# Kernel tuning notes

Hardware: AMD Instinct MI355X
Metric: run time of the kernel (lower is better)

The kernel has to match this reference:

```python
import jax, jax.numpy as jnp
import numpy as np

EPS = 1e-06


def setup_inputs() -> dict:
    key = jax.random.key(0)
    kx, kw, kb = jax.random.split(key, 3)
    C = 128
    x = jax.random.normal(kx, (8, C, 256, 256), dtype=jnp.float32)
    # 1x1 conv weights: [C_out, C_in]
    W = jax.random.normal(kw, (C, C), dtype=jnp.float32) * (1.0 / np.sqrt(C))
    b = jax.random.normal(kb, (C,), dtype=jnp.float32) * 0.01
    return {"x": x, "W": W, "b": b}


def reference(x, W, b):
    # torch.std_mean over channel dim (dim=1), std is unbiased (ddof=1)
    u = jnp.mean(x, axis=1, keepdims=True)                  # [B,1,H,W]
    var = jnp.var(x, axis=1, keepdims=True, ddof=1)         # unbiased
    s = jnp.sqrt(var)
    n_x = (x - u) / (s + EPS)
    # 1x1 conv == pointwise GEMM over channels
    n_x = jnp.einsum('bchw,oc->bohw', n_x, W) + b[None, :, None, None]
    return x * n_x
```

## Files before the change

kernel.cpp:

```cpp
#include <hip/hip_runtime.h>

#define EPS 1e-6f

constexpr int C    = 128;
constexpr int HW   = 65536;
constexpr int TILE = 128;
constexpr int NT   = 512;

typedef __attribute__((ext_vector_type(8))) short bf16x8;
typedef __attribute__((ext_vector_type(4))) float f32x4;

__device__ __forceinline__ unsigned short f2bf(float f) {
    unsigned u = __float_as_uint(f);
    u += 0x7fff + ((u >> 16) & 1);
    return (unsigned short)(u >> 16);
}
__device__ __forceinline__ float bf2f(unsigned short u) {
    return __uint_as_float(((unsigned)u) << 16);
}
__device__ __forceinline__ unsigned pack2(float lo, float hi) {
    return (unsigned)f2bf(lo) | ((unsigned)f2bf(hi) << 16);
}

__global__ __launch_bounds__(NT, 4) void spnorm_kernel(
    const float* __restrict__ x, const float* __restrict__ W,
    const float* __restrict__ bias, float* __restrict__ out)
{
    __shared__ unsigned short bufT[C * TILE];
    __shared__ float red1[4][TILE], red2[4][TILE];
    __shared__ float u_s[TILE], se_s[TILE];

    const int tid = threadIdx.x;
    const int l   = tid & 63;
    const int wv  = tid >> 6;
    const int batch = blockIdx.x >> 9;
    const int hw0   = (blockIdx.x & 511) * TILE;
    const int base  = batch * (C * HW) + hw0;

    const int p = tid & 127;
    const int q = tid >> 7;

    float v[32];
    {
        const float* xp = x + base + q * 32 * HW + p;
        #pragma unroll
        for (int i = 0; i < 32; ++i)
            v[i] = xp[i * HW];
    }

    const int arow  = (wv << 4) + (l & 15);
    const int acol0 = (l >> 4) << 3;
    bf16x8 afrag[4];
    #pragma unroll
    for (int kk = 0; kk < 4; ++kk) {
        const float* wp = W + arow * C + kk * 32 + acol0;
        float4 wa = *reinterpret_cast<const float4*>(wp);
        float4 wb = *reinterpret_cast<const float4*>(wp + 4);
        bf16x8 f;
        f[0] = (short)f2bf(wa.x); f[1] = (short)f2bf(wa.y);
        f[2] = (short)f2bf(wa.z); f[3] = (short)f2bf(wa.w);
        f[4] = (short)f2bf(wb.x); f[5] = (short)f2bf(wb.y);
        f[6] = (short)f2bf(wb.z); f[7] = (short)f2bf(wb.w);
        afrag[kk] = f;
    }
    const int od = (wv << 4) + ((l >> 4) << 2);
    const f32x4 binit = { bias[od], bias[od + 1], bias[od + 2], bias[od + 3] };

    {
        float s1 = 0.f, s2 = 0.f;
        #pragma unroll
        for (int i = 0; i < 32; ++i) {
            s1 += v[i];
            s2 = fmaf(v[i], v[i], s2);
        }
        red1[q][p] = s1;
        red2[q][p] = s2;
    }
    __syncthreads();

    {
        float s1 = red1[0][p] + red1[1][p] + red1[2][p] + red1[3][p];
        float s2 = red2[0][p] + red2[1][p] + red2[2][p] + red2[3][p];
        float u   = s1 * (1.0f / 128.0f);
        float var = fmaxf((s2 - s1 * u) * (1.0f / 127.0f), 0.0f);
        float se  = sqrtf(var) + EPS;
        float iv  = 1.0f / se;
        if (q == 0) {
            u_s[p]  = u;
            se_s[p] = se;
        }
        char* tb = (char*)bufT;
        const int rowoff = p * 256;
        const int swz    = (p & 15) << 4;
        #pragma unroll
        for (int o8 = 0; o8 < 4; ++o8) {
            float n0 = (v[o8 * 8 + 0] - u) * iv;
            float n1 = (v[o8 * 8 + 1] - u) * iv;
            float n2 = (v[o8 * 8 + 2] - u) * iv;
            float n3 = (v[o8 * 8 + 3] - u) * iv;
            float n4 = (v[o8 * 8 + 4] - u) * iv;
            float n5 = (v[o8 * 8 + 5] - u) * iv;
            float n6 = (v[o8 * 8 + 6] - u) * iv;
            float n7 = (v[o8 * 8 + 7] - u) * iv;
            uint4 d;
            d.x = pack2(n0, n1);
            d.y = pack2(n2, n3);
            d.z = pack2(n4, n5);
            d.w = pack2(n6, n7);
            int byte = (rowoff + (q * 4 + o8) * 16) ^ swz;
            *reinterpret_cast<uint4*>(tb + byte) = d;
        }
    }
    __syncthreads();

    {
        const char* tb = (const char*)bufT;
        const int pcol = l & 15;
        const int koff = (l >> 4) << 4;
        const int swz  = pcol << 4;
        float* outp = out + base;
        #pragma unroll
        for (int pt = 0; pt < 8; ++pt) {
            const int pp     = (pt << 4) + pcol;
            const int rowoff = pp * 256;
            f32x4 acc = binit;
            #pragma unroll
            for (int kk = 0; kk < 4; ++kk) {
                int byte = (rowoff + kk * 64 + koff) ^ swz;
                bf16x8 bfrag = *reinterpret_cast<const bf16x8*>(tb + byte);
                acc = __builtin_amdgcn_mfma_f32_16x16x32_bf16(afrag[kk], bfrag, acc, 0, 0, 0);
            }
            const float uu = u_s[pp];
            const float se = se_s[pp];
            int nbyte = (rowoff + od * 2) ^ swz;
            uint2 nn = *reinterpret_cast<const uint2*>(tb + nbyte);
            float x0 = fmaf(bf2f((unsigned short)(nn.x & 0xffffu)), se, uu);
            float x1 = fmaf(bf2f((unsigned short)(nn.x >> 16)),     se, uu);
            float x2 = fmaf(bf2f((unsigned short)(nn.y & 0xffffu)), se, uu);
            float x3 = fmaf(bf2f((unsigned short)(nn.y >> 16)),     se, uu);
            outp[(od + 0) * HW + pp] = x0 * acc[0];
            outp[(od + 1) * HW + pp] = x1 * acc[1];
            outp[(od + 2) * HW + pp] = x2 * acc[2];
            outp[(od + 3) * HW + pp] = x3 * acc[3];
        }
    }
}

extern "C" void kernel_launch(void* const* d_in, const int* in_sizes, int n_in,
                              void* d_out, int out_size, void* d_ws, size_t ws_size,
                              hipStream_t stream) {
    const float* x = (const float*)d_in[0];
    const float* W = (const float*)d_in[1];
    const float* b = (const float*)d_in[2];
    float* out     = (float*)d_out;

    const int nblk = 8 * HW / TILE;
    spnorm_kernel<<<nblk, NT, 0, stream>>>(x, W, b, out);
}
```

Before: 121.3 us.

## Halve pixel tile to 64 with 256 threads, each wave computing two output blocks

Shrinks the per-block pixel tile from 128 to 64 and the block from 512 to 256 threads, doubling the grid and raising occupancy (launch bounds now request 8 blocks). Each wave now covers 32 output channels with two MFMA accumulators sharing one B-fragment load. The W fragment loads move after the normalisation stage to lower peak register pressure, and the two reduction arrays merge into one float2 array. Smaller tiles mean W is loaded and converted more often per pixel, and global store coalescing runs are shorter (64 contiguous floats).

```diff
diff --git a/kernel.cpp b/kernel.cpp
--- a/kernel.cpp
+++ b/kernel.cpp
@@ -4,8 +4,8 @@
 
 constexpr int C    = 128;
 constexpr int HW   = 65536;
-constexpr int TILE = 128;
-constexpr int NT   = 512;
+constexpr int TILE = 64;
+constexpr int NT   = 256;
 
 typedef __attribute__((ext_vector_type(8))) short bf16x8;
 typedef __attribute__((ext_vector_type(4))) float f32x4;
@@ -22,23 +22,23 @@
     return (unsigned)f2bf(lo) | ((unsigned)f2bf(hi) << 16);
 }
 
-__global__ __launch_bounds__(NT, 4) void spnorm_kernel(
+__global__ __launch_bounds__(NT, 8) void spnorm_kernel(
     const float* __restrict__ x, const float* __restrict__ W,
     const float* __restrict__ bias, float* __restrict__ out)
 {
-    __shared__ unsigned short bufT[C * TILE];
-    __shared__ float red1[4][TILE], red2[4][TILE];
+    __shared__ unsigned short bufT[TILE * C];
+    __shared__ float2 red[4][TILE];
     __shared__ float u_s[TILE], se_s[TILE];
 
     const int tid = threadIdx.x;
     const int l   = tid & 63;
     const int wv  = tid >> 6;
-    const int batch = blockIdx.x >> 9;
-    const int hw0   = (blockIdx.x & 511) * TILE;
+    const int batch = blockIdx.x >> 10;
+    const int hw0   = (blockIdx.x & 1023) * TILE;
     const int base  = batch * (C * HW) + hw0;
 
-    const int p = tid & 127;
-    const int q = tid >> 7;
+    const int p = l;
+    const int q = wv;
 
     float v[32];
     {
@@ -48,24 +48,6 @@
             v[i] = xp[i * HW];
     }
 
-    const int arow  = (wv << 4) + (l & 15);
-    const int acol0 = (l >> 4) << 3;
-    bf16x8 afrag[4];
-    #pragma unroll
-    for (int kk = 0; kk < 4; ++kk) {
-        const float* wp = W + arow * C + kk * 32 + acol0;
-        float4 wa = *reinterpret_cast<const float4*>(wp);
-        float4 wb = *reinterpret_cast<const float4*>(wp + 4);
-        bf16x8 f;
-        f[0] = (short)f2bf(wa.x); f[1] = (short)f2bf(wa.y);
-        f[2] = (short)f2bf(wa.z); f[3] = (short)f2bf(wa.w);
-        f[4] = (short)f2bf(wb.x); f[5] = (short)f2bf(wb.y);
-        f[6] = (short)f2bf(wb.z); f[7] = (short)f2bf(wb.w);
-        afrag[kk] = f;
-    }
-    const int od = (wv << 4) + ((l >> 4) << 2);
-    const f32x4 binit = { bias[od], bias[od + 1], bias[od + 2], bias[od + 3] };
-
     {
         float s1 = 0.f, s2 = 0.f;
         #pragma unroll
@@ -73,14 +55,14 @@
             s1 += v[i];
             s2 = fmaf(v[i], v[i], s2);
         }
-        red1[q][p] = s1;
-        red2[q][p] = s2;
+        red[q][p] = make_float2(s1, s2);
     }
     __syncthreads();
 
     {
-        float s1 = red1[0][p] + red1[1][p] + red1[2][p] + red1[3][p];
-        float s2 = red2[0][p] + red2[1][p] + red2[2][p] + red2[3][p];
+        float2 r0 = red[0][p], r1 = red[1][p], r2 = red[2][p], r3 = red[3][p];
+        float s1 = r0.x + r1.x + r2.x + r3.x;
+        float s2 = r0.y + r1.y + r2.y + r3.y;
         float u   = s1 * (1.0f / 128.0f);
         float var = fmaxf((s2 - s1 * u) * (1.0f / 127.0f), 0.0f);
         float se  = sqrtf(var) + EPS;
@@ -111,6 +93,29 @@
             *reinterpret_cast<uint4*>(tb + byte) = d;
         }
     }
+
+    const int odr = (l >> 4) << 2;
+    bf16x8 afrag[2][4];
+    f32x4 binit[2];
+    #pragma unroll
+    for (int ob = 0; ob < 2; ++ob) {
+        const int arow = (wv << 5) + (ob << 4) + (l & 15);
+        const int acol0 = (l >> 4) << 3;
+        #pragma unroll
+        for (int kk = 0; kk < 4; ++kk) {
+            const float* wp = W + arow * C + kk * 32 + acol0;
+            float4 wa = *reinterpret_cast<const float4*>(wp);
+            float4 wb = *reinterpret_cast<const float4*>(wp + 4);
+            bf16x8 f;
+            f[0] = (short)f2bf(wa.x); f[1] = (short)f2bf(wa.y);
+            f[2] = (short)f2bf(wa.z); f[3] = (short)f2bf(wa.w);
+            f[4] = (short)f2bf(wb.x); f[5] = (short)f2bf(wb.y);
+            f[6] = (short)f2bf(wb.z); f[7] = (short)f2bf(wb.w);
+            afrag[ob][kk] = f;
+        }
+        const int od = (wv << 5) + (ob << 4) + odr;
+        binit[ob] = f32x4{ bias[od], bias[od + 1], bias[od + 2], bias[od + 3] };
+    }
     __syncthreads();
 
     {
@@ -119,29 +124,49 @@
         const int koff = (l >> 4) << 4;
         const int swz  = pcol << 4;
         float* outp = out + base;
+
         #pragma unroll
-        for (int pt = 0; pt < 8; ++pt) {
+        for (int pt = 0; pt < 4; ++pt) {
             const int pp     = (pt << 4) + pcol;
             const int rowoff = pp * 256;
-            f32x4 acc = binit;
+            f32x4 acc0 = binit[0];
+            f32x4 acc1 = binit[1];
             #pragma unroll
             for (int kk = 0; kk < 4; ++kk) {
                 int byte = (rowoff + kk * 64 + koff) ^ swz;
                 bf16x8 bfrag = *reinterpret_cast<const bf16x8*>(tb + byte);
-                acc = __builtin_amdgcn_mfma_f32_16x16x32_bf16(afrag[kk], bfrag, acc, 0, 0, 0);
+                acc0 = __builtin_amdgcn_mfma_f32_16x16x32_bf16(afrag[0][kk], bfrag, acc0, 0, 0, 0);
+                acc1 = __builtin_amdgcn_mfma_f32_16x16x32_bf16(afrag[1][kk], bfrag, acc1, 0, 0, 0);
             }
             const float uu = u_s[pp];
             const float se = se_s[pp];
-            int nbyte = (rowoff + od * 2) ^ swz;
-            uint2 nn = *reinterpret_cast<const uint2*>(tb + nbyte);
-            float x0 = fmaf(bf2f((unsigned short)(nn.x & 0xffffu)), se, uu);
-            float x1 = fmaf(bf2f((unsigned short)(nn.x >> 16)),     se, uu);
-            float x2 = fmaf(bf2f((unsigned short)(nn.y & 0xffffu)), se, uu);
-            float x3 = fmaf(bf2f((unsigned short)(nn.y >> 16)),     se, uu);
-            outp[(od + 0) * HW + pp] = x0 * acc[0];
-            outp[(od + 1) * HW + pp] = x1 * acc[1];
-            outp[(od + 2) * HW + pp] = x2 * acc[2];
-            outp[(od + 3) * HW + pp] = x3 * acc[3];
+
+            {
+                const int od = (wv << 5) + odr;
+                int nbyte = (rowoff + od * 2) ^ swz;
+                uint2 nn = *reinterpret_cast<const uint2*>(tb + nbyte);
+                float x0 = fmaf(bf2f((unsigned short)(nn.x & 0xffffu)), se, uu);
+                float x1 = fmaf(bf2f((unsigned short)(nn.x >> 16)),     se, uu);
+                float x2 = fmaf(bf2f((unsigned short)(nn.y & 0xffffu)), se, uu);
+                float x3 = fmaf(bf2f((unsigned short)(nn.y >> 16)),     se, uu);
+                outp[(od + 0) * HW + pp] = x0 * acc0[0];
+                outp[(od + 1) * HW + pp] = x1 * acc0[1];
+                outp[(od + 2) * HW + pp] = x2 * acc0[2];
+                outp[(od + 3) * HW + pp] = x3 * acc0[3];
+            }
+            {
+                const int od = (wv << 5) + 16 + odr;
+                int nbyte = (rowoff + od * 2) ^ swz;
+                uint2 nn = *reinterpret_cast<const uint2*>(tb + nbyte);
+                float x0 = fmaf(bf2f((unsigned short)(nn.x & 0xffffu)), se, uu);
+                float x1 = fmaf(bf2f((unsigned short)(nn.x >> 16)),     se, uu);
+                float x2 = fmaf(bf2f((unsigned short)(nn.y & 0xffffu)), se, uu);
+                float x3 = fmaf(bf2f((unsigned short)(nn.y >> 16)),     se, uu);
+                outp[(od + 0) * HW + pp] = x0 * acc1[0];
+                outp[(od + 1) * HW + pp] = x1 * acc1[1];
+                outp[(od + 2) * HW + pp] = x2 * acc1[2];
+                outp[(od + 3) * HW + pp] = x3 * acc1[3];
+            }
         }
     }
 }
```

Result: slower. 424.5 us (+249.9%).
